# Kernel tuning notes

Measured on AMD Instinct MI355X. Metric: run time of the kernel, lower is better.

The kernel has to match this reference:

```python
import jax, jax.numpy as jnp
import numpy as np

B = 4096
D = 1024
WEIGHT = 1.0
EPS = 1e-7  # Keras K.epsilon()


def setup_inputs() -> dict:
    key = jax.random.key(0)
    k1, k2 = jax.random.split(key)
    return {
        "left": jax.random.normal(k1, (B, D), dtype=jnp.float32),
        "right": jax.random.normal(k2, (B, D), dtype=jnp.float32),
        "temperature": jnp.zeros((1,), dtype=jnp.float32),
    }


def _l2_normalize(x):
    # matches l2_norm: sqrt(max(sum(x^2), eps))
    sq = jnp.sum(jnp.square(x), axis=-1, keepdims=True)
    return x / jnp.sqrt(jnp.maximum(sq, EPS))


def reference(left, right, temperature):
    ln = _l2_normalize(left)   # [B, D]
    rn = _l2_normalize(right)  # [B, D]
    scale = jnp.exp(temperature)  # (1,) broadcasts
    logits_left = jnp.einsum("bd,cd->bc", ln, rn) * scale   # [B, B]
    logits_right = logits_left.T                             # rn @ ln.T * scale
    prob_left = jax.nn.softmax(logits_left, axis=-1)
    prob_right = jax.nn.softmax(logits_right, axis=-1)
    # NOTE: the original calls CCE(prob, labels), i.e. y_true=prob, y_pred=eye.
    # Keras clips y_pred to [eps, 1-eps]; loss = -sum(y_true * log(clip(y_pred))).
    labels = jnp.eye(B, dtype=jnp.float32)
    log_clipped = jnp.log(jnp.clip(labels, EPS, 1.0 - EPS))  # diag: log(1-eps), off: log(eps)
    loss_left = -jnp.sum(prob_left * log_clipped)
    loss_right = -jnp.sum(prob_right * log_clipped)
    loss = (loss_left + loss_right) / 2.0 / B
    return WEIGHT * loss
```

## Files before the change

kernel.cpp:

```cpp
#include <hip/hip_runtime.h>
#include <hip/hip_bf16.h>

#define Bn 4096
#define Dk 1024
#define EPSF 1e-7f

typedef float f32x4 __attribute__((ext_vector_type(4)));
typedef long long2_t __attribute__((ext_vector_type(2)));

__device__ __forceinline__ void async_copy16(const void* g, void* l) {
    __builtin_amdgcn_global_load_lds((__attribute__((address_space(1))) void*)(uintptr_t)g,
                                     (__attribute__((address_space(3))) void*)l, 16, 0, 0);
}

__global__ __launch_bounds__(256)
void nrm_kernel(const float4* __restrict__ left, const float4* __restrict__ right,
                unsigned char* __restrict__ lnb8, unsigned char* __restrict__ rnb8,
                float* __restrict__ diag, float* __restrict__ rowsum,
                float* __restrict__ colsum)
{
    const int row = blockIdx.x;
    const int t = threadIdx.x;
    const int idx = row * (Dk / 4) + t;
    const float4 l = left[idx];
    const float4 r = right[idx];
    float sl = l.x * l.x + l.y * l.y + l.z * l.z + l.w * l.w;
    float sr = r.x * r.x + r.y * r.y + r.z * r.z + r.w * r.w;
    float slr = l.x * r.x + l.y * r.y + l.z * r.z + l.w * r.w;
    #pragma unroll
    for (int off = 1; off < 64; off <<= 1) {
        sl += __shfl_xor(sl, off);
        sr += __shfl_xor(sr, off);
        slr += __shfl_xor(slr, off);
    }
    __shared__ float red[3][4];
    const int wave = t >> 6, lane = t & 63;
    if (lane == 0) { red[0][wave] = sl; red[1][wave] = sr; red[2][wave] = slr; }
    __syncthreads();
    sl = red[0][0] + red[0][1] + red[0][2] + red[0][3];
    sr = red[1][0] + red[1][1] + red[1][2] + red[1][3];
    const float invl = 1.0f / sqrtf(fmaxf(sl, EPSF));
    const float invr = 1.0f / sqrtf(fmaxf(sr, EPSF));
    const float sL = 8.0f * invl;
    const float sR = 8.0f * invr;
    int pkL = __builtin_amdgcn_cvt_pk_fp8_f32(l.x * sL, l.y * sL, 0, false);
    pkL = __builtin_amdgcn_cvt_pk_fp8_f32(l.z * sL, l.w * sL, pkL, true);
    int pkR = __builtin_amdgcn_cvt_pk_fp8_f32(r.x * sR, r.y * sR, 0, false);
    pkR = __builtin_amdgcn_cvt_pk_fp8_f32(r.z * sR, r.w * sR, pkR, true);
    const int k0 = 4 * t;
    const int g = k0 >> 6;
    const int kl = k0 & 63;
    const int dst = row * Dk + (g << 6) + (((kl & 31) >> 3) << 4) + ((kl >> 5) << 3) + (kl & 7);
    *(unsigned*)(lnb8 + dst) = (unsigned)pkL;
    *(unsigned*)(rnb8 + dst) = (unsigned)pkR;
    if (t == 0) {
        const float d = red[2][0] + red[2][1] + red[2][2] + red[2][3];
        diag[row] = d * invl * invr;
        rowsum[row] = 0.f;
        colsum[row] = 0.f;
    }
}

__global__ __launch_bounds__(256, 3)
void gemm_sm_kernel(const unsigned char* __restrict__ lnb8,
                    const unsigned char* __restrict__ rnb8,
                    const float* __restrict__ temp,
                    float* __restrict__ rowsum, float* __restrict__ colsum)
{
    __shared__ __align__(16) unsigned char As[2][128 * 64];
    __shared__ __align__(16) unsigned char Bs[2][128 * 64];

    const int tid = threadIdx.x;
    const int wave = tid >> 6;
    const int lane = tid & 63;
    const int bm0 = blockIdx.y * 128;
    const int bn0 = blockIdx.x * 128;

    const int srow = lane >> 2;
    const int sj = lane & 3;
    int goff[2];
    int lofs[2];
    #pragma unroll
    for (int i = 0; i < 2; ++i) {
        const int rloc = wave * 32 + i * 16 + srow;
        goff[i] = rloc * Dk + 16 * (sj ^ ((rloc >> 1) & 3));
        lofs[i] = (wave * 32 + i * 16) * 64;
    }
    const unsigned char* baseA = lnb8 + (size_t)bm0 * Dk;
    const unsigned char* baseB = rnb8 + (size_t)bn0 * Dk;

    const int wm = (wave & 1) * 64;
    const int wn = (wave >> 1) * 64;
    const int quad = lane >> 4;
    const int r16 = lane & 15;
    const int skey = (r16 >> 1) & 3;
    int aoff[4], boff[4];
    #pragma unroll
    for (int i = 0; i < 4; ++i) {
        aoff[i] = (wm + i * 16 + r16) * 64 + 16 * (quad ^ skey);
        boff[i] = (wn + i * 16 + r16) * 64 + 16 * (quad ^ skey);
    }

    f32x4 acc[4][4];
    #pragma unroll
    for (int i = 0; i < 4; ++i)
        #pragma unroll
        for (int j = 0; j < 4; ++j)
            acc[i][j] = (f32x4){0.f, 0.f, 0.f, 0.f};

    #pragma unroll
    for (int i = 0; i < 2; ++i) {
        async_copy16(baseA + goff[i], &As[0][lofs[i]]);
        async_copy16(baseB + goff[i], &Bs[0][lofs[i]]);
    }

    #pragma unroll 2
    for (int it = 0; it < 16; ++it) {
        const int cur = it & 1;
        const int nxt = cur ^ 1;
        const int knext = ((it + 1) & 15) * 64;
        #pragma unroll
        for (int i = 0; i < 2; ++i) {
            async_copy16(baseA + goff[i] + knext, &As[nxt][lofs[i]]);
            async_copy16(baseB + goff[i] + knext, &Bs[nxt][lofs[i]]);
        }
        asm volatile("s_waitcnt vmcnt(4)\n\ts_barrier" ::: "memory");
        long2_t af01[4], bf01[4];
        #pragma unroll
        for (int i = 0; i < 4; ++i) af01[i] = *(const long2_t*)(&As[cur][aoff[i]]);
        #pragma unroll
        for (int i = 0; i < 4; ++i) bf01[i] = *(const long2_t*)(&Bs[cur][boff[i]]);
        #pragma unroll
        for (int mi = 0; mi < 4; ++mi)
            #pragma unroll
            for (int ni = 0; ni < 4; ++ni)
                acc[mi][ni] = __builtin_amdgcn_mfma_f32_16x16x32_fp8_fp8(
                    af01[mi].x, bf01[ni].x, acc[mi][ni], 0, 0, 0);
        #pragma unroll
        for (int mi = 0; mi < 4; ++mi)
            #pragma unroll
            for (int ni = 0; ni < 4; ++ni)
                acc[mi][ni] = __builtin_amdgcn_mfma_f32_16x16x32_fp8_fp8(
                    af01[mi].y, bf01[ni].y, acc[mi][ni], 0, 0, 0);
        asm volatile("s_barrier" ::: "memory");
    }

    const float scale = __expf(temp[0]);
    const float dq = 0.015625f * scale;
    #pragma unroll
    for (int mi = 0; mi < 4; ++mi)
        #pragma unroll
        for (int ni = 0; ni < 4; ++ni)
            #pragma unroll
            for (int r = 0; r < 4; ++r)
                acc[mi][ni][r] = __expf(dq * acc[mi][ni][r] - scale);

    #pragma unroll
    for (int mi = 0; mi < 4; ++mi) {
        #pragma unroll
        for (int r = 0; r < 4; ++r) {
            float v = acc[mi][0][r] + acc[mi][1][r] + acc[mi][2][r] + acc[mi][3][r];
            v += __shfl_xor(v, 1);
            v += __shfl_xor(v, 2);
            v += __shfl_xor(v, 4);
            v += __shfl_xor(v, 8);
            if (r16 == 0)
                atomicAdd(&rowsum[bm0 + wm + mi * 16 + quad * 4 + r], v);
        }
    }
    #pragma unroll
    for (int ni = 0; ni < 4; ++ni) {
        float v = 0.f;
        #pragma unroll
        for (int mi = 0; mi < 4; ++mi)
            #pragma unroll
            for (int r = 0; r < 4; ++r)
                v += acc[mi][ni][r];
        v += __shfl_xor(v, 16);
        v += __shfl_xor(v, 32);
        if (quad == 0)
            atomicAdd(&colsum[bn0 + wn + ni * 16 + r16], v);
    }
}

__global__ __launch_bounds__(256)
void loss_kernel(const float* __restrict__ diag, const float* __restrict__ rowsum,
                 const float* __restrict__ colsum, const float* __restrict__ temp,
                 float* __restrict__ out)
{
    const int t = threadIdx.x;
    const float scale = __expf(temp[0]);
    float dL = 0.f, dR = 0.f;
    for (int i = t; i < Bn; i += 256) {
        const float e = __expf(scale * (diag[i] - 1.0f));
        dL += e * __builtin_amdgcn_rcpf(rowsum[i]);
        dR += e * __builtin_amdgcn_rcpf(colsum[i]);
    }
    #pragma unroll
    for (int off = 1; off < 64; off <<= 1) {
        dL += __shfl_xor(dL, off);
        dR += __shfl_xor(dR, off);
    }
    __shared__ float rd[2][4];
    const int wave = t >> 6, lane = t & 63;
    if (lane == 0) { rd[0][wave] = dL; rd[1][wave] = dR; }
    __syncthreads();
    if (t == 0) {
        dL = rd[0][0] + rd[0][1] + rd[0][2] + rd[0][3];
        dR = rd[1][0] + rd[1][1] + rd[1][2] + rd[1][3];
        const float logeps = logf(EPSF);
        const float log1m = logf(1.0f - EPSF);
        const float lossL = -(dL * log1m + ((float)Bn - dL) * logeps);
        const float lossR = -(dR * log1m + ((float)Bn - dR) * logeps);
        out[0] = (lossL + lossR) * 0.5f / (float)Bn;
    }
}

extern "C" void kernel_launch(void* const* d_in, const int* in_sizes, int n_in,
                              void* d_out, int out_size, void* d_ws, size_t ws_size,
                              hipStream_t stream) {
    (void)in_sizes; (void)n_in; (void)out_size; (void)ws_size;
    const float* left = (const float*)d_in[0];
    const float* right = (const float*)d_in[1];
    const float* temp = (const float*)d_in[2];

    char* ws = (char*)d_ws;
    unsigned char* lnb8 = (unsigned char*)ws;
    unsigned char* rnb8 = (unsigned char*)(ws + (size_t)Bn * Dk);
    float* diag = (float*)(ws + 2 * (size_t)Bn * Dk);
    float* rowsum = diag + Bn;
    float* colsum = rowsum + Bn;

    nrm_kernel<<<Bn, 256, 0, stream>>>((const float4*)left, (const float4*)right,
                                       lnb8, rnb8, diag, rowsum, colsum);
    dim3 g2(Bn / 128, Bn / 128);
    gemm_sm_kernel<<<g2, 256, 0, stream>>>(lnb8, rnb8, temp, rowsum, colsum);
    loss_kernel<<<1, 256, 0, stream>>>(diag, rowsum, colsum, temp, (float*)d_out);
}
```

Before: 115.8 us.

## Split GEMM tile across eight waves with dedicated A/B staging waves

Doubles the GEMM block to 512 threads (8 waves) over the same 128x128 tile. Each wave now computes a 32x64 sub-tile, and the staging work is split so that waves 0-3 load A and waves 4-7 load B. This halves the accumulators and MFMAs per wave, which should improve latency hiding and occupancy. In exchange it doubles the LDS fragment reads of B across waves and adds more barrier participants.

```diff
diff --git a/kernel.cpp b/kernel.cpp
--- a/kernel.cpp
+++ b/kernel.cpp
@@ -61,7 +61,7 @@
     }
 }
 
-__global__ __launch_bounds__(256, 3)
+__global__ __launch_bounds__(512, 4)
 void gemm_sm_kernel(const unsigned char* __restrict__ lnb8,
                     const unsigned char* __restrict__ rnb8,
                     const float* __restrict__ temp,
@@ -78,40 +78,44 @@
 
     const int srow = lane >> 2;
     const int sj = lane & 3;
-    int goff[2];
-    int lofs[2];
+    const int swcol = 16 * (sj ^ ((srow >> 1) & 3));
+    const bool stagesA = (wave < 4);
+    const unsigned char* sbase = stagesA ? (lnb8 + (size_t)bm0 * Dk)
+                                         : (rnb8 + (size_t)bn0 * Dk);
+    const int rb = (wave & 3) * 32;
+    int goff[2], lofs[2];
     #pragma unroll
     for (int i = 0; i < 2; ++i) {
-        const int rloc = wave * 32 + i * 16 + srow;
-        goff[i] = rloc * Dk + 16 * (sj ^ ((rloc >> 1) & 3));
-        lofs[i] = (wave * 32 + i * 16) * 64;
-    }
-    const unsigned char* baseA = lnb8 + (size_t)bm0 * Dk;
-    const unsigned char* baseB = rnb8 + (size_t)bn0 * Dk;
-
-    const int wm = (wave & 1) * 64;
-    const int wn = (wave >> 1) * 64;
+        goff[i] = (rb + i * 16 + srow) * Dk + swcol;
+        lofs[i] = (rb + i * 16) * 64;
+    }
+
+    const int wm = (wave & 3) * 32;
+    const int wn = (wave >> 2) * 64;
     const int quad = lane >> 4;
     const int r16 = lane & 15;
     const int skey = (r16 >> 1) & 3;
-    int aoff[4], boff[4];
-    #pragma unroll
-    for (int i = 0; i < 4; ++i) {
-        aoff[i] = (wm + i * 16 + r16) * 64 + 16 * (quad ^ skey);
-        boff[i] = (wn + i * 16 + r16) * 64 + 16 * (quad ^ skey);
-    }
-
-    f32x4 acc[4][4];
+    const int gq = 16 * (quad ^ skey);
+    int aoff[2], boff[4];
+    #pragma unroll
+    for (int i = 0; i < 2; ++i)
+        aoff[i] = (wm + i * 16 + r16) * 64 + gq;
     #pragma unroll
     for (int i = 0; i < 4; ++i)
+        boff[i] = (wn + i * 16 + r16) * 64 + gq;
+
+    f32x4 acc[2][4];
+    #pragma unroll
+    for (int i = 0; i < 2; ++i)
         #pragma unroll
         for (int j = 0; j < 4; ++j)
             acc[i][j] = (f32x4){0.f, 0.f, 0.f, 0.f};
 
-    #pragma unroll
-    for (int i = 0; i < 2; ++i) {
-        async_copy16(baseA + goff[i], &As[0][lofs[i]]);
-        async_copy16(baseB + goff[i], &Bs[0][lofs[i]]);
+    {
+        unsigned char* dst0 = stagesA ? &As[0][0] : &Bs[0][0];
+        #pragma unroll
+        for (int i = 0; i < 2; ++i)
+            async_copy16(sbase + goff[i], dst0 + lofs[i]);
     }
 
     #pragma unroll 2
@@ -119,25 +123,24 @@
         const int cur = it & 1;
         const int nxt = cur ^ 1;
         const int knext = ((it + 1) & 15) * 64;
-        #pragma unroll
-        for (int i = 0; i < 2; ++i) {
-            async_copy16(baseA + goff[i] + knext, &As[nxt][lofs[i]]);
-            async_copy16(baseB + goff[i] + knext, &Bs[nxt][lofs[i]]);
-        }
-        asm volatile("s_waitcnt vmcnt(4)\n\ts_barrier" ::: "memory");
-        long2_t af01[4], bf01[4];
-        #pragma unroll
-        for (int i = 0; i < 4; ++i) af01[i] = *(const long2_t*)(&As[cur][aoff[i]]);
+        unsigned char* dst = stagesA ? &As[nxt][0] : &Bs[nxt][0];
+        #pragma unroll
+        for (int i = 0; i < 2; ++i)
+            async_copy16(sbase + goff[i] + knext, dst + lofs[i]);
+        asm volatile("s_waitcnt vmcnt(2)\n\ts_barrier" ::: "memory");
+        long2_t af01[2], bf01[4];
+        #pragma unroll
+        for (int i = 0; i < 2; ++i) af01[i] = *(const long2_t*)(&As[cur][aoff[i]]);
         #pragma unroll
         for (int i = 0; i < 4; ++i) bf01[i] = *(const long2_t*)(&Bs[cur][boff[i]]);
         #pragma unroll
-        for (int mi = 0; mi < 4; ++mi)
+        for (int mi = 0; mi < 2; ++mi)
             #pragma unroll
             for (int ni = 0; ni < 4; ++ni)
                 acc[mi][ni] = __builtin_amdgcn_mfma_f32_16x16x32_fp8_fp8(
                     af01[mi].x, bf01[ni].x, acc[mi][ni], 0, 0, 0);
         #pragma unroll
-        for (int mi = 0; mi < 4; ++mi)
+        for (int mi = 0; mi < 2; ++mi)
             #pragma unroll
             for (int ni = 0; ni < 4; ++ni)
                 acc[mi][ni] = __builtin_amdgcn_mfma_f32_16x16x32_fp8_fp8(
@@ -148,7 +151,7 @@
     const float scale = __expf(temp[0]);
     const float dq = 0.015625f * scale;
     #pragma unroll
-    for (int mi = 0; mi < 4; ++mi)
+    for (int mi = 0; mi < 2; ++mi)
         #pragma unroll
         for (int ni = 0; ni < 4; ++ni)
             #pragma unroll
@@ -156,10 +159,12 @@
                 acc[mi][ni][r] = __expf(dq * acc[mi][ni][r] - scale);
 
     #pragma unroll
-    for (int mi = 0; mi < 4; ++mi) {
+    for (int mi = 0; mi < 2; ++mi) {
         #pragma unroll
         for (int r = 0; r < 4; ++r) {
-            float v = acc[mi][0][r] + acc[mi][1][r] + acc[mi][2][r] + acc[mi][3][r];
+            float v = 0.f;
+            #pragma unroll
+            for (int ni = 0; ni < 4; ++ni) v += acc[mi][ni][r];
             v += __shfl_xor(v, 1);
             v += __shfl_xor(v, 2);
             v += __shfl_xor(v, 4);
@@ -172,7 +177,7 @@
     for (int ni = 0; ni < 4; ++ni) {
         float v = 0.f;
         #pragma unroll
-        for (int mi = 0; mi < 4; ++mi)
+        for (int mi = 0; mi < 2; ++mi)
             #pragma unroll
             for (int r = 0; r < 4; ++r)
                 v += acc[mi][ni][r];
@@ -234,6 +239,6 @@
     nrm_kernel<<<Bn, 256, 0, stream>>>((const float4*)left, (const float4*)right,
                                        lnb8, rnb8, diag, rowsum, colsum);
     dim3 g2(Bn / 128, Bn / 128);
-    gemm_sm_kernel<<<g2, 256, 0, stream>>>(lnb8, rnb8, temp, rowsum, colsum);
+    gemm_sm_kernel<<<g2, 512, 0, stream>>>(lnb8, rnb8, temp, rowsum, colsum);
     loss_kernel<<<1, 256, 0, stream>>>(diag, rowsum, colsum, temp, (float*)d_out);
 }
```

New measurement: 119.0 us. +2.8%, slower.
